# Optimization experiments

Hardware: AMD Instinct MI355X
Metric: run time of the kernel (lower is better)

## Reference

```python
import jax, jax.numpy as jnp
import numpy as np

P = 1_500_000
N_DEPTH = 6 * 118 * 16 * 44  # 498432 flattened depth bins
N_FEAT = 6 * 16 * 44         # 4224 flattened feature rows
TOTAL_BEV = 40000            # 200x200 BEV grid
C = 80


def setup_inputs() -> dict:
    key = jax.random.key(0)
    k1, k2, k3, k4, k5, k6, k7 = jax.random.split(key, 7)
    depth = jax.random.uniform(k1, (6, 118, 16, 44), dtype=jnp.float32)
    feat = jax.random.normal(k2, (6, 16, 44, C), dtype=jnp.float32)
    ranks_depth = jax.random.randint(k3, (P,), 0, N_DEPTH, dtype=jnp.int64)
    ranks_feat = jax.random.randint(k4, (P,), 0, N_FEAT, dtype=jnp.int64)
    ranks_bev = jnp.sort(jax.random.randint(k5, (P,), 0, TOTAL_BEV, dtype=jnp.int64))
    interval_starts = jnp.sort(jax.random.randint(k6, (TOTAL_BEV,), 0, P, dtype=jnp.int64))
    interval_lengths = jax.random.randint(k7, (TOTAL_BEV,), 0, 64, dtype=jnp.int64)
    return {
        "depth": depth,
        "feat": feat,
        "ranks_depth": ranks_depth,
        "ranks_feat": ranks_feat,
        "ranks_bev": ranks_bev,
        "interval_starts": interval_starts,
        "interval_lengths": interval_lengths,
        "total_bev": TOTAL_BEV,
    }


def reference(depth, feat, ranks_depth, ranks_feat, ranks_bev,
              interval_starts, interval_lengths, total_bev):
    # interval_starts / interval_lengths are unused (as in the torch source)
    channels = feat.shape[-1]
    feat_flat = feat.reshape(-1, channels).astype(jnp.float32)   # [N_feat, C]
    depth_flat = depth.reshape(-1).astype(jnp.float32)           # [N_depth]
    gathered_feat = feat_flat[ranks_feat]                        # [P, C]
    gathered_depth = depth_flat[ranks_depth][:, None]            # [P, 1]
    weighted_feat = gathered_feat * gathered_depth               # [P, C]
    out = jax.ops.segment_sum(weighted_feat, ranks_bev,
                              num_segments=int(total_bev))       # [total_bev, C]
    return out
```

## Files before the change

kernel.cpp:

```cpp
#include <hip/hip_runtime.h>


#define CHN 80

__global__ __launch_bounds__(256)
void seg_starts_kernel(const int* __restrict__ rb, int* __restrict__ seg,
                       int P, int total_bev) {
    int q = blockIdx.x * blockDim.x + threadIdx.x;
    int i4 = q * 4;
    if (i4 >= P) return;
    const int4 v = *reinterpret_cast<const int4*>(rb + i4);
    int prev = (i4 == 0) ? -1 : rb[i4 - 1];
    int cur;
    cur = v.x; for (int b = prev + 1; b <= cur; ++b) seg[b] = i4 + 0; prev = cur;
    cur = v.y; for (int b = prev + 1; b <= cur; ++b) seg[b] = i4 + 1; prev = cur;
    cur = v.z; for (int b = prev + 1; b <= cur; ++b) seg[b] = i4 + 2; prev = cur;
    cur = v.w; for (int b = prev + 1; b <= cur; ++b) seg[b] = i4 + 3; prev = cur;
    if (i4 + 4 >= P) {
        for (int b = prev + 1; b <= total_bev; ++b) seg[b] = P;
    }
}

__global__ __launch_bounds__(256)
void bev_pool_kernel(const float* __restrict__ depth,
                     const float* __restrict__ feat,
                     const int* __restrict__ rd,
                     const int* __restrict__ rf,
                     const int* __restrict__ seg,
                     float* __restrict__ out,
                     int total_bev) {
    const int wave = threadIdx.x >> 6;
    const int lane = threadIdx.x & 63;
    const int bin = blockIdx.x * 4 + wave;
    if (bin >= total_bev) return;

    const int slot = lane / 20;
    const int l    = lane % 20;
    const int c    = l * 4;

    const int lo = seg[bin];
    const int hi = seg[bin + 1];

    float4 acc = make_float4(0.f, 0.f, 0.f, 0.f);

    int i = lo + slot;
    bool valid = (slot < 3) && (i < hi);
    int di = 0, fi = 0;
    if (valid) { di = rd[i]; fi = rf[i]; }
    while (valid) {
        const int ni = i + 3;
        const bool nvalid = ni < hi;
        int ndi = 0, nfi = 0;
        if (nvalid) { ndi = rd[ni]; nfi = rf[ni]; }
        const float d  = depth[di];
        const float4 f = *reinterpret_cast<const float4*>(feat + (size_t)fi * CHN + c);
        acc.x += d * f.x;
        acc.y += d * f.y;
        acc.z += d * f.z;
        acc.w += d * f.w;
        i = ni; di = ndi; fi = nfi; valid = nvalid;
    }

    const float sx1 = __shfl(acc.x, lane + 20, 64);
    const float sy1 = __shfl(acc.y, lane + 20, 64);
    const float sz1 = __shfl(acc.z, lane + 20, 64);
    const float sw1 = __shfl(acc.w, lane + 20, 64);
    const float sx2 = __shfl(acc.x, lane + 40, 64);
    const float sy2 = __shfl(acc.y, lane + 40, 64);
    const float sz2 = __shfl(acc.z, lane + 40, 64);
    const float sw2 = __shfl(acc.w, lane + 40, 64);
    acc.x += sx1 + sx2;
    acc.y += sy1 + sy2;
    acc.z += sz1 + sz2;
    acc.w += sw1 + sw2;

    if (lane < 20) {
        *reinterpret_cast<float4*>(out + (size_t)bin * CHN + c) = acc;
    }
}

extern "C" void kernel_launch(void* const* d_in, const int* in_sizes, int n_in,
                              void* d_out, int out_size, void* d_ws, size_t ws_size,
                              hipStream_t stream) {
    const float* depth = (const float*)d_in[0];
    const float* feat  = (const float*)d_in[1];
    const int*   rd    = (const int*)d_in[2];
    const int*   rf    = (const int*)d_in[3];
    const int*   rb    = (const int*)d_in[4];
    float* out = (float*)d_out;

    const int P = in_sizes[2];
    const int total_bev = out_size / CHN;

    int* seg = (int*)d_ws;

    const int quads = (P + 3) / 4;
    seg_starts_kernel<<<(quads + 255) / 256, 256, 0, stream>>>(rb, seg, P, total_bev);
    bev_pool_kernel<<<(total_bev + 3) / 4, 256, 0, stream>>>(depth, feat, rd, rf, seg,
                                                             out, total_bev);
}
```

Baseline: 129.6 us.

## Process 16 points per wave with 4 lanes per feature row

After: 119.4 us. 7.9% less time.

```diff
diff --git a/kernel.cpp b/kernel.cpp
--- a/kernel.cpp
+++ b/kernel.cpp
@@ -34,48 +34,63 @@
     const int bin = blockIdx.x * 4 + wave;
     if (bin >= total_bev) return;
 
-    const int slot = lane / 20;
-    const int l    = lane % 20;
-    const int c    = l * 4;
+    const int slot = lane >> 2;
+    const int ll   = lane & 3;
 
     const int lo = seg[bin];
     const int hi = seg[bin + 1];
 
-    float4 acc = make_float4(0.f, 0.f, 0.f, 0.f);
+    float4 a0 = make_float4(0.f, 0.f, 0.f, 0.f);
+    float4 a1 = a0, a2 = a0, a3 = a0, a4 = a0;
 
     int i = lo + slot;
-    bool valid = (slot < 3) && (i < hi);
+    bool valid = i < hi;
     int di = 0, fi = 0;
     if (valid) { di = rd[i]; fi = rf[i]; }
     while (valid) {
-        const int ni = i + 3;
+        const int ni = i + 16;
         const bool nvalid = ni < hi;
         int ndi = 0, nfi = 0;
         if (nvalid) { ndi = rd[ni]; nfi = rf[ni]; }
-        const float d  = depth[di];
-        const float4 f = *reinterpret_cast<const float4*>(feat + (size_t)fi * CHN + c);
-        acc.x += d * f.x;
-        acc.y += d * f.y;
-        acc.z += d * f.z;
-        acc.w += d * f.w;
+
+        const float d = depth[di];
+        const float4* frow = reinterpret_cast<const float4*>(feat + (size_t)fi * CHN) + ll;
+        const float4 f0 = frow[0];
+        const float4 f1 = frow[4];
+        const float4 f2 = frow[8];
+        const float4 f3 = frow[12];
+        const float4 f4 = frow[16];
+        a0.x += d * f0.x; a0.y += d * f0.y; a0.z += d * f0.z; a0.w += d * f0.w;
+        a1.x += d * f1.x; a1.y += d * f1.y; a1.z += d * f1.z; a1.w += d * f1.w;
+        a2.x += d * f2.x; a2.y += d * f2.y; a2.z += d * f2.z; a2.w += d * f2.w;
+        a3.x += d * f3.x; a3.y += d * f3.y; a3.z += d * f3.z; a3.w += d * f3.w;
+        a4.x += d * f4.x; a4.y += d * f4.y; a4.z += d * f4.z; a4.w += d * f4.w;
+
         i = ni; di = ndi; fi = nfi; valid = nvalid;
     }
 
-    const float sx1 = __shfl(acc.x, lane + 20, 64);
-    const float sy1 = __shfl(acc.y, lane + 20, 64);
-    const float sz1 = __shfl(acc.z, lane + 20, 64);
-    const float sw1 = __shfl(acc.w, lane + 20, 64);
-    const float sx2 = __shfl(acc.x, lane + 40, 64);
-    const float sy2 = __shfl(acc.y, lane + 40, 64);
-    const float sz2 = __shfl(acc.z, lane + 40, 64);
-    const float sw2 = __shfl(acc.w, lane + 40, 64);
-    acc.x += sx1 + sx2;
-    acc.y += sy1 + sy2;
-    acc.z += sz1 + sz2;
-    acc.w += sw1 + sw2;
+    #pragma unroll
+    for (int ofs = 4; ofs <= 32; ofs <<= 1) {
+        a0.x += __shfl_xor(a0.x, ofs, 64); a0.y += __shfl_xor(a0.y, ofs, 64);
+        a0.z += __shfl_xor(a0.z, ofs, 64); a0.w += __shfl_xor(a0.w, ofs, 64);
+        a1.x += __shfl_xor(a1.x, ofs, 64); a1.y += __shfl_xor(a1.y, ofs, 64);
+        a1.z += __shfl_xor(a1.z, ofs, 64); a1.w += __shfl_xor(a1.w, ofs, 64);
+        a2.x += __shfl_xor(a2.x, ofs, 64); a2.y += __shfl_xor(a2.y, ofs, 64);
+        a2.z += __shfl_xor(a2.z, ofs, 64); a2.w += __shfl_xor(a2.w, ofs, 64);
+        a3.x += __shfl_xor(a3.x, ofs, 64); a3.y += __shfl_xor(a3.y, ofs, 64);
+        a3.z += __shfl_xor(a3.z, ofs, 64); a3.w += __shfl_xor(a3.w, ofs, 64);
+        a4.x += __shfl_xor(a4.x, ofs, 64); a4.y += __shfl_xor(a4.y, ofs, 64);
+        a4.z += __shfl_xor(a4.z, ofs, 64); a4.w += __shfl_xor(a4.w, ofs, 64);
+    }
 
     if (lane < 20) {
-        *reinterpret_cast<float4*>(out + (size_t)bin * CHN + c) = acc;
+        const int j = lane >> 2;
+        float4 w = a0;
+        if (j == 1) w = a1;
+        else if (j == 2) w = a2;
+        else if (j == 3) w = a3;
+        else if (j == 4) w = a4;
+        *reinterpret_cast<float4*>(out + (size_t)bin * CHN + lane * 4) = w;
     }
 }
 
```
